# Performance work log

Hardware: AMD Instinct MI355X
Metric: run time of the kernel (lower is better)

Reference implementation:

```python
import jax, jax.numpy as jnp
import numpy as np

NUM_USERS = 1_000_000
NUM_ITEMS = 1_000_000
HIDDEN = 64
BATCH = 1_048_576


def setup_inputs() -> dict:
    key = jax.random.key(0)
    k_uw, k_iw, k_u, k_i, k_t = jax.random.split(key, 5)
    return {
        "user": jax.random.randint(k_u, (BATCH,), 0, NUM_USERS, dtype=jnp.int32),
        "item": jax.random.randint(k_i, (BATCH,), 0, NUM_ITEMS, dtype=jnp.int32),
        "target": jax.random.uniform(k_t, (BATCH,), dtype=jnp.float32),
        "user_weight": 0.01 * jax.random.normal(k_uw, (NUM_USERS, HIDDEN), dtype=jnp.float32),
        "item_weight": 0.01 * jax.random.normal(k_iw, (NUM_ITEMS, HIDDEN), dtype=jnp.float32),
        "user_bias": jnp.zeros((NUM_USERS, 1), dtype=jnp.float32),
        "item_bias": jnp.zeros((NUM_ITEMS, 1), dtype=jnp.float32),
        "bias": jnp.zeros((1,), dtype=jnp.float32),
    }


def reference(user, item, target, user_weight, item_weight, user_bias, item_bias, bias):
    # user_embedding = user_weight[u] + user_bias[u]  (bias [1] broadcasts over hidden)
    u_emb = user_weight[user] + user_bias[user]  # [B, H]
    i_emb = item_weight[item] + item_bias[item]  # [B, H]
    pred = jnp.sum(u_emb * i_emb, axis=-1) + bias[0]  # [B]
    return pred
```

## Files before the change

kernel.cpp:

```cpp
#include <hip/hip_runtime.h>


__global__ __launch_bounds__(256) void MF_73856257622285_kernel(
    const int*   __restrict__ user,
    const int*   __restrict__ item,
    const float* __restrict__ user_weight,
    const float* __restrict__ item_weight,
    const float* __restrict__ user_bias,
    const float* __restrict__ item_bias,
    const float* __restrict__ bias,
    float*       __restrict__ out,
    int batch)
{
    const int lane16 = threadIdx.x & 15;
    const int grp    = threadIdx.x >> 4;
    const int row0   = blockIdx.x * 64 + grp;

    int u[4], it[4];
    bool ok[4];
    #pragma unroll
    for (int k = 0; k < 4; ++k) {
        const int r = row0 + k * 16;
        ok[k] = r < batch;
        u[k]  = ok[k] ? user[r] : 0;
        it[k] = ok[k] ? item[r] : 0;
    }

    float4 uw[4], iw[4];
    #pragma unroll
    for (int k = 0; k < 4; ++k) {
        uw[k] = ((const float4*)(user_weight + (size_t)u[k]  * 64))[lane16];
        iw[k] = ((const float4*)(item_weight + (size_t)it[k] * 64))[lane16];
    }

    float ub[4], ib[4];
    #pragma unroll
    for (int k = 0; k < 4; ++k) {
        ub[k] = user_bias[u[k]];
        ib[k] = item_bias[it[k]];
    }

    const float b0 = bias[0];

    float s[4];
    #pragma unroll
    for (int k = 0; k < 4; ++k) {
        s[k] = (uw[k].x + ub[k]) * (iw[k].x + ib[k])
             + (uw[k].y + ub[k]) * (iw[k].y + ib[k])
             + (uw[k].z + ub[k]) * (iw[k].z + ib[k])
             + (uw[k].w + ub[k]) * (iw[k].w + ib[k]);
    }

    #pragma unroll
    for (int off = 8; off >= 1; off >>= 1) {
        #pragma unroll
        for (int k = 0; k < 4; ++k) s[k] += __shfl_xor(s[k], off, 16);
    }

    if (lane16 == 0) {
        #pragma unroll
        for (int k = 0; k < 4; ++k) {
            if (ok[k]) __builtin_nontemporal_store(s[k] + b0, &out[row0 + k * 16]);
        }
    }
}

extern "C" void kernel_launch(void* const* d_in, const int* in_sizes, int n_in,
                              void* d_out, int out_size, void* d_ws, size_t ws_size,
                              hipStream_t stream) {
    const int*   user        = (const int*)  d_in[0];
    const int*   item        = (const int*)  d_in[1];
    const float* user_weight = (const float*)d_in[3];
    const float* item_weight = (const float*)d_in[4];
    const float* user_bias   = (const float*)d_in[5];
    const float* item_bias   = (const float*)d_in[6];
    const float* bias        = (const float*)d_in[7];
    float*       out         = (float*)d_out;

    const int batch = in_sizes[0];

    const int threads = 256;
    const int rows_per_block = 64;
    const int blocks = (batch + rows_per_block - 1) / rows_per_block;

    MF_73856257622285_kernel<<<blocks, threads, 0, stream>>>(
        user, item, user_weight, item_weight, user_bias, item_bias, bias,
        out, batch);
}
```

Measured before the change: 503.6 us.

## Bucket-sort batch rows by user id before gathering embeddings

Adds a histogram, scan and scatter pipeline that groups batch rows into 1024 buckets by high bits of the user index, then computes predictions per bucket and scatters results back to original positions. The aim is to make user-embedding gathers within a block hit a narrow slice of the user table, improving cache locality. It costs four extra launches, global atomics on bucket cursors, extra traffic for the sorted index arrays, and scattered output writes. Item gathers stay random and buckets are processed by only 1024 blocks. It falls back to the original kernel when the workspace is too small.

```diff
diff --git a/kernel.cpp b/kernel.cpp
--- a/kernel.cpp
+++ b/kernel.cpp
@@ -1,5 +1,148 @@
 #include <hip/hip_runtime.h>
 
+
+#define NBUCKET 1024
+#define BSHIFT  10
+
+__global__ __launch_bounds__(1024) void mf_zero(int* __restrict__ counts)
+{
+    counts[threadIdx.x] = 0;
+}
+
+__global__ __launch_bounds__(1024) void mf_hist(const int* __restrict__ user,
+                                                int batch,
+                                                int* __restrict__ counts)
+{
+    __shared__ int lc[NBUCKET];
+    for (int i = threadIdx.x; i < NBUCKET; i += blockDim.x) lc[i] = 0;
+    __syncthreads();
+    for (int i = blockIdx.x * blockDim.x + threadIdx.x; i < batch;
+         i += gridDim.x * blockDim.x)
+        atomicAdd(&lc[user[i] >> BSHIFT], 1);
+    __syncthreads();
+    for (int i = threadIdx.x; i < NBUCKET; i += blockDim.x) {
+        const int c = lc[i];
+        if (c) atomicAdd(&counts[i], c);
+    }
+}
+
+__global__ __launch_bounds__(1024) void mf_scan(const int* __restrict__ counts,
+                                                int* __restrict__ offsets,
+                                                int* __restrict__ cursor)
+{
+    const int t    = threadIdx.x;
+    const int lane = t & 63;
+    const int wid  = t >> 6;
+
+    const int v = counts[t];
+    int x = v;
+    #pragma unroll
+    for (int off = 1; off < 64; off <<= 1) {
+        const int y = __shfl_up(x, off, 64);
+        if (lane >= off) x += y;
+    }
+    __shared__ int wsum[16], wpre[16];
+    if (lane == 63) wsum[wid] = x;
+    __syncthreads();
+    if (t == 0) {
+        int s = 0;
+        for (int w = 0; w < 16; ++w) { wpre[w] = s; s += wsum[w]; }
+    }
+    __syncthreads();
+    const int excl = x - v + wpre[wid];
+    offsets[t] = excl;
+    cursor[t]  = excl;
+    if (t == NBUCKET - 1) offsets[NBUCKET] = excl + v;
+}
+
+__global__ __launch_bounds__(256) void mf_scatter(const int* __restrict__ user,
+                                                  const int* __restrict__ item,
+                                                  int batch,
+                                                  int* __restrict__ cursor,
+                                                  int* __restrict__ s_user,
+                                                  int* __restrict__ s_item,
+                                                  int* __restrict__ s_pos)
+{
+    for (int i = blockIdx.x * blockDim.x + threadIdx.x; i < batch;
+         i += gridDim.x * blockDim.x) {
+        const int u  = user[i];
+        const int it = item[i];
+        const int slot = atomicAdd(&cursor[u >> BSHIFT], 1);
+        s_user[slot] = u;
+        s_item[slot] = it;
+        s_pos[slot]  = i;
+    }
+}
+
+__global__ __launch_bounds__(256) void mf_bucket_compute(
+    const int*   __restrict__ s_user,
+    const int*   __restrict__ s_item,
+    const int*   __restrict__ s_pos,
+    const int*   __restrict__ offsets,
+    const float* __restrict__ user_weight,
+    const float* __restrict__ item_weight,
+    const float* __restrict__ user_bias,
+    const float* __restrict__ item_bias,
+    const float* __restrict__ bias,
+    float*       __restrict__ out)
+{
+    const int start = offsets[blockIdx.x];
+    const int end   = offsets[blockIdx.x + 1];
+    if (start >= end) return;
+
+    const int lane16 = threadIdx.x & 15;
+    const int grp    = threadIdx.x >> 4;
+    const float b0   = bias[0];
+
+    for (int base = start; base < end; base += 64) {
+        int u[4], it[4], pos[4];
+        bool ok[4];
+        #pragma unroll
+        for (int k = 0; k < 4; ++k) {
+            const int r  = base + grp + k * 16;
+            ok[k]        = r < end;
+            const int rr = ok[k] ? r : start;
+            u[k]   = s_user[rr];
+            it[k]  = s_item[rr];
+            pos[k] = s_pos[rr];
+        }
+
+        float4 uw[4], iw[4];
+        #pragma unroll
+        for (int k = 0; k < 4; ++k) {
+            uw[k] = ((const float4*)(user_weight + (size_t)u[k]  * 64))[lane16];
+            iw[k] = ((const float4*)(item_weight + (size_t)it[k] * 64))[lane16];
+        }
+
+        float ub[4], ib[4];
+        #pragma unroll
+        for (int k = 0; k < 4; ++k) {
+            ub[k] = user_bias[u[k]];
+            ib[k] = item_bias[it[k]];
+        }
+
+        float s[4];
+        #pragma unroll
+        for (int k = 0; k < 4; ++k) {
+            s[k] = (uw[k].x + ub[k]) * (iw[k].x + ib[k])
+                 + (uw[k].y + ub[k]) * (iw[k].y + ib[k])
+                 + (uw[k].z + ub[k]) * (iw[k].z + ib[k])
+                 + (uw[k].w + ub[k]) * (iw[k].w + ib[k]);
+        }
+
+        #pragma unroll
+        for (int off = 8; off >= 1; off >>= 1) {
+            #pragma unroll
+            for (int k = 0; k < 4; ++k) s[k] += __shfl_xor(s[k], off, 16);
+        }
+
+        if (lane16 == 0) {
+            #pragma unroll
+            for (int k = 0; k < 4; ++k)
+                if (ok[k]) out[pos[k]] = s[k] + b0;
+        }
+    }
+}
 
 __global__ __launch_bounds__(256) void MF_73856257622285_kernel(
     const int*   __restrict__ user,
@@ -67,7 +210,10 @@
 
 extern "C" void kernel_launch(void* const* d_in, const int* in_sizes, int n_in,
                               void* d_out, int out_size, void* d_ws, size_t ws_size,
-                              hipStream_t stream) {
+                              hipStream_t stream)
+{
+    (void)n_in; (void)out_size;
+
     const int*   user        = (const int*)  d_in[0];
     const int*   item        = (const int*)  d_in[1];
     const float* user_weight = (const float*)d_in[3];
@@ -78,12 +224,33 @@
     float*       out         = (float*)d_out;
 
     const int batch = in_sizes[0];
-
-    const int threads = 256;
-    const int rows_per_block = 64;
-    const int blocks = (batch + rows_per_block - 1) / rows_per_block;
-
-    MF_73856257622285_kernel<<<blocks, threads, 0, stream>>>(
-        user, item, user_weight, item_weight, user_bias, item_bias, bias,
-        out, batch);
-}
+    if (batch <= 0) return;
+
+    const size_t need = (size_t)(3 * NBUCKET + 1) * sizeof(int)
+                      + (size_t)batch * 3 * sizeof(int);
+
+    if (d_ws != nullptr && ws_size >= need) {
+        int* counts  = (int*)d_ws;
+        int* offsets = counts  + NBUCKET;
+        int* cursor  = offsets + NBUCKET + 1;
+        int* s_user  = cursor  + NBUCKET;
+        int* s_item  = s_user  + batch;
+        int* s_pos   = s_item  + batch;
+
+        mf_zero<<<1, NBUCKET, 0, stream>>>(counts);
+        mf_hist<<<64, 1024, 0, stream>>>(user, batch, counts);
+        mf_scan<<<1, NBUCKET, 0, stream>>>(counts, offsets, cursor);
+        mf_scatter<<<1024, 256, 0, stream>>>(user, item, batch, cursor,
+                                             s_user, s_item, s_pos);
+        mf_bucket_compute<<<NBUCKET, 256, 0, stream>>>(
+            s_user, s_item, s_pos, offsets,
+            user_weight, item_weight, user_bias, item_bias, bias, out);
+    } else {
+        const int threads = 256;
+        const int rows_per_block = 64;
+        const int blocks = (batch + rows_per_block - 1) / rows_per_block;
+        MF_73856257622285_kernel<<<blocks, threads, 0, stream>>>(
+            user, item, user_weight, item_weight, user_bias, item_bias, bias,
+            out, batch);
+    }
+}
```

New measurement: 739.4 us. 46.8% more time.
